# Optimization experiments

Hardware: AMD Instinct MI355X
Metric: run time of the kernel (lower is better)

## Reference

```python
import jax, jax.numpy as jnp
import numpy as np

N = 8192
IN_F = 512
OUT_F = 512
ALPHA = 0.2  # leaky relu slope


def setup_inputs() -> dict:
    key = jax.random.key(0)
    k1, k2, k3, k4, k5 = jax.random.split(key, 5)
    inp = jax.random.normal(k1, (N, IN_F), dtype=jnp.float32)
    adj = jax.random.randint(k2, (N, N), 0, 2, dtype=jnp.int32)
    # linear1: [in, out] + bias
    W1 = jax.random.normal(k3, (IN_F, OUT_F), dtype=jnp.float32) * (1.0 / np.sqrt(IN_F))
    b1 = jnp.zeros((OUT_F,), dtype=jnp.float32)
    # linear2: maps 2*out -> 1; split into the two halves acting on h_i and h_j
    a = jax.random.normal(k4, (2 * OUT_F,), dtype=jnp.float32) * (1.0 / np.sqrt(2 * OUT_F))
    a1 = a[:OUT_F]
    a2 = a[OUT_F:]
    b2 = jnp.zeros((), dtype=jnp.float32)
    return {"inp": inp, "adj": adj, "W1": W1, "b1": b1, "a1": a1, "a2": a2, "b2": b2}


def reference(inp, adj, W1, b1, a1, a2, b2):
    h = inp @ W1 + b1  # [N, out]
    # linear2(cat(h_i, h_j)) == h_i@a1 + h_j@a2 + b2 -> avoids the N*N*2F tensor
    e = jax.nn.leaky_relu((h @ a1)[:, None] + (h @ a2)[None, :] + b2, ALPHA)  # [N, N]
    attention = jnp.where(adj > 0, e, jnp.float32(-1e12))
    attention = jax.nn.softmax(attention, axis=1)
    h_prime = attention @ h  # [N, out]
    return jax.nn.elu(h_prime)  # concat=True
```

## Files before the change

kernel.cpp:

```cpp
#include <hip/hip_runtime.h>
#include <hip/hip_bf16.h>
#include <stdint.h>

#define NR 8192
#define FD 512
#define BM 128
#define BKC 128

typedef __attribute__((ext_vector_type(8))) short s8v;
typedef __attribute__((ext_vector_type(4))) float f32x4;

static __device__ __forceinline__ short bf16_rtne(float x) {
    union { float f; uint32_t u; } v; v.f = x;
    uint32_t r = (v.u + 0x7FFFu + ((v.u >> 16) & 1u)) >> 16;
    return (short)r;
}
static __device__ __forceinline__ float bf16_to_f32(short s) {
    union { uint32_t u; float f; } v; v.u = ((uint32_t)(uint16_t)s) << 16;
    return v.f;
}
static __device__ __forceinline__ float asfloat_u32(uint32_t u) {
    union { uint32_t u; float f; } v; v.u = u; return v.f;
}

__global__ void k_prepack(const int* __restrict__ adj, uint32_t* __restrict__ bm) {
    int t = blockIdx.x * 256 + threadIdx.x;
    const int4* p = (const int4*)(adj + (size_t)t * 32);
    uint32_t word = 0;
#pragma unroll
    for (int g = 0; g < 8; ++g) {
        int4 v = p[g];
        word |= (uint32_t)(v.x != 0) << (g * 4);
        word |= (uint32_t)(v.y != 0) << (g * 4 + 1);
        word |= (uint32_t)(v.z != 0) << (g * 4 + 2);
        word |= (uint32_t)(v.w != 0) << (g * 4 + 3);
    }
    bm[t] = word;
}

__global__ void k_convert(const float* __restrict__ in, short* __restrict__ out) {
    int i = blockIdx.x * blockDim.x + threadIdx.x;
    float4 v = ((const float4*)in)[i];
    short4 s;
    s.x = bf16_rtne(v.x); s.y = bf16_rtne(v.y);
    s.z = bf16_rtne(v.z); s.w = bf16_rtne(v.w);
    ((short4*)out)[i] = s;
}

__global__ void k_w1t(const float* __restrict__ W1, short* __restrict__ W1T) {
    int i = blockIdx.x * 256 + threadIdx.x;
    int k = i & 511, n = i >> 9;
    W1T[(size_t)n * 512 + k] = bf16_rtne(W1[(size_t)k * 512 + n]);
}

__launch_bounds__(256)
__global__ void k_gemm_h(const short* __restrict__ A,
                         const short* __restrict__ BT,
                         const float* __restrict__ b1,
                         short* __restrict__ H,
                         short* __restrict__ HT2)
{
    const int lane = threadIdx.x & 63;
    const int wn   = threadIdx.x >> 6;
    const int m    = lane & 15;
    const int q    = lane >> 4;
    const int r0   = blockIdx.x * 32;
    const int c0   = blockIdx.y * 128 + wn * 32;

    f32x4 acc[2][2] = {};
#pragma unroll 1
    for (int k0 = 0; k0 < 512; k0 += 32) {
        s8v a[2], b[2];
#pragma unroll
        for (int rt = 0; rt < 2; ++rt)
            a[rt] = *(const s8v*)(A + (size_t)(r0 + rt * 16 + m) * 512 + k0 + q * 8);
#pragma unroll
        for (int nt = 0; nt < 2; ++nt)
            b[nt] = *(const s8v*)(BT + (size_t)(c0 + nt * 16 + m) * 512 + k0 + q * 8);
#pragma unroll
        for (int rt = 0; rt < 2; ++rt)
#pragma unroll
            for (int nt = 0; nt < 2; ++nt)
                acc[rt][nt] = __builtin_amdgcn_mfma_f32_16x16x32_bf16(a[rt], b[nt], acc[rt][nt], 0, 0, 0);
    }
    float b1v[2];
#pragma unroll
    for (int nt = 0; nt < 2; ++nt) b1v[nt] = b1[c0 + nt * 16 + m];

#pragma unroll
    for (int rt = 0; rt < 2; ++rt)
#pragma unroll
        for (int nt = 0; nt < 2; ++nt) {
            int col = c0 + nt * 16 + m;
            short4 hp;
#pragma unroll
            for (int r = 0; r < 4; ++r) {
                int row = r0 + rt * 16 + q * 4 + r;
                short hv = bf16_rtne(acc[rt][nt][r] + b1v[nt]);
                H[(size_t)row * 512 + col] = hv;
                ((short*)&hp)[r] = hv;
            }
            *(short4*)(HT2 + (size_t)blockIdx.x * (512 * 32) + (size_t)col * 32 + rt * 16 + q * 4) = hp;
        }
}

__global__ void k_f1f2(const short* __restrict__ H, const float* __restrict__ a1,
                       const float* __restrict__ a2, const float* __restrict__ b2,
                       float* __restrict__ nf1, float* __restrict__ E1,
                       float* __restrict__ E1b, uint2* __restrict__ jtab)
{
    const int lane = threadIdx.x & 63;
    const int row  = blockIdx.x * 4 + (threadIdx.x >> 6);
    s8v hv = *(const s8v*)(H + (size_t)row * 512 + lane * 8);
    float4 a1l = ((const float4*)(a1 + lane * 8))[0];
    float4 a1h = ((const float4*)(a1 + lane * 8))[1];
    float4 a2l = ((const float4*)(a2 + lane * 8))[0];
    float4 a2h = ((const float4*)(a2 + lane * 8))[1];
    float hf[8];
#pragma unroll
    for (int i = 0; i < 8; ++i) hf[i] = bf16_to_f32(hv[i]);
    float s1 = hf[0] * a1l.x + hf[1] * a1l.y + hf[2] * a1l.z + hf[3] * a1l.w
             + hf[4] * a1h.x + hf[5] * a1h.y + hf[6] * a1h.z + hf[7] * a1h.w;
    float s2 = hf[0] * a2l.x + hf[1] * a2l.y + hf[2] * a2l.z + hf[3] * a2l.w
             + hf[4] * a2h.x + hf[5] * a2h.y + hf[6] * a2h.z + hf[7] * a2h.w;
#pragma unroll
    for (int o = 32; o > 0; o >>= 1) {
        s1 += __shfl_xor(s1, o);
        s2 += __shfl_xor(s2, o);
    }
    if (lane == 0) {
        float f1v = s1;
        float f2v = s2 + b2[0];
        nf1[row]  = -f1v;
        E1[row]   = __expf(f1v);
        E1b[row]  = __expf(0.2f * f1v);
        uint32_t p = (uint32_t)(uint16_t)bf16_rtne(__expf(f2v))
                   | ((uint32_t)(uint16_t)bf16_rtne(__expf(0.2f * f2v)) << 16);
        union { float f; uint32_t u; } fb; fb.f = f2v;
        jtab[row] = make_uint2(p, fb.u);
    }
}

__launch_bounds__(512, 4)
__global__ void k_attn(const uint32_t* __restrict__ bm,
                       const short* __restrict__ HT2,
                       const float* __restrict__ nf1,
                       const float* __restrict__ E1,
                       const float* __restrict__ E1b,
                       const uint2* __restrict__ jtab,
                       float* __restrict__ nump,
                       float* __restrict__ denomp)
{
    __shared__ __align__(16) short wt[2][BM * BKC];

    const int t    = threadIdx.x;
    const int lane = t & 63;
    const int w    = t >> 6;
    const int wm   = w & 1;
    const int wn   = w >> 1;
    const int m    = lane & 15;
    const int q    = lane >> 4;

    const int band = blockIdx.x >> 3;
    const int cb   = (blockIdx.x >> 1) & 3;
    const int js   = blockIdx.x & 1;
    const int r0   = band * BM;
    const int jsb  = js * 4096;

    const int rowq = t >> 4;
    const int jg   = t & 15;
    const int byteoff = (jg & 3) * 8;

    float nf1v[4], e1v[4], e1bv[4];
#pragma unroll
    for (int r = 0; r < 4; ++r) {
        int rr = r0 + rowq * 4 + r;
        nf1v[r] = nf1[rr]; e1v[r] = E1[rr]; e1bv[r] = E1b[rr];
    }
    const uint32_t* bmp = bm + (size_t)(r0 + rowq * 4) * 256 + (jsb >> 5) + (jg >> 2);
    const uint4*   tabp = (const uint4*)jtab + ((jsb + jg * 8) >> 1);

    const int colbase = cb * 128 + wn * 32;
    const short* htp = HT2 + (size_t)(jsb >> 5) * 16384 + q * 8;

    f32x4 acc[4][2] = {};
    float dsum[4] = {0.f, 0.f, 0.f, 0.f};

#pragma unroll 1
    for (int ch = 0; ch < 4096 / BKC; ++ch) {
        const int p = ch & 1;
        uint32_t bw[4];
#pragma unroll
        for (int r = 0; r < 4; ++r) bw[r] = bmp[(size_t)r * 256 + ch * 4];
        uint4 tb[4];
#pragma unroll
        for (int i = 0; i < 4; ++i) tb[i] = tabp[ch * 64 + i];
        const uint32_t* tw = (const uint32_t*)tb;

#pragma unroll
        for (int r = 0; r < 4; ++r) {
            uint32_t byte = (bw[r] >> byteoff) & 0xFFu;
            s8v wv;
            float ds = 0.f;
#pragma unroll
            for (int jj = 0; jj < 8; ++jj) {
                uint32_t pk  = tw[jj * 2];
                float e2  = asfloat_u32(pk << 16);
                float e2b = asfloat_u32(pk & 0xFFFF0000u);
                float f2  = asfloat_u32(tw[jj * 2 + 1]);
                bool  c   = (f2 >= nf1v[r]);
                float wgt = c ? (e1v[r] * e2) : (e1bv[r] * e2b);
                wgt = ((byte >> jj) & 1u) ? wgt : 0.f;
                ds += wgt;
                wv[jj] = bf16_rtne(wgt);
            }
            dsum[r] += ds;
            int row  = rowq * 4 + r;
            int slot = jg ^ (row & 15);
            *(s8v*)&wt[p][row * BKC + slot * 8] = wv;
        }

        __syncthreads();

#pragma unroll
        for (int kk = 0; kk < 4; ++kk) {
            s8v b[2];
#pragma unroll
            for (int nt = 0; nt < 2; ++nt)
                b[nt] = *(const s8v*)(htp + (size_t)(ch * 4 + kk) * 16384 + (colbase + nt * 16 + m) * 32);
            const int sb = kk * 4 + q;
            s8v af[4];
#pragma unroll
            for (int i = 0; i < 4; ++i) {
                int row = wm * 64 + i * 16 + m;
                af[i] = *(const s8v*)&wt[p][row * BKC + ((sb ^ m) << 3)];
            }
#pragma unroll
            for (int i = 0; i < 4; ++i)
#pragma unroll
                for (int nt = 0; nt < 2; ++nt)
                    acc[i][nt] = __builtin_amdgcn_mfma_f32_16x16x32_bf16(af[i], b[nt], acc[i][nt], 0, 0, 0);
        }
    }

#pragma unroll
    for (int r = 0; r < 4; ++r) {
#pragma unroll
        for (int o = 1; o < 16; o <<= 1) dsum[r] += __shfl_xor(dsum[r], o);
    }
    if (cb == 0 && jg == 0) {
#pragma unroll
        for (int r = 0; r < 4; ++r)
            denomp[(size_t)js * NR + r0 + rowq * 4 + r] = dsum[r];
    }

    float* np = nump + (size_t)js * NR * FD;
#pragma unroll
    for (int i = 0; i < 4; ++i)
#pragma unroll
        for (int nt = 0; nt < 2; ++nt)
#pragma unroll
            for (int r = 0; r < 4; ++r) {
                int row = r0 + wm * 64 + i * 16 + q * 4 + r;
                int col = colbase + nt * 16 + m;
                np[(size_t)row * FD + col] = acc[i][nt][r];
            }
}

__global__ void k_combine(const float* __restrict__ nump,
                          const float* __restrict__ denomp,
                          float* __restrict__ out)
{
    size_t e = ((size_t)blockIdx.x * 256 + threadIdx.x) * 4;
    int row = (int)(e >> 9);
    float4 n0 = *(const float4*)(nump + e);
    float4 n1 = *(const float4*)(nump + (size_t)NR * FD + e);
    float d = denomp[row] + denomp[NR + row];
    float inv = 1.0f / d;
    float4 o;
    o.x = (n0.x + n1.x) * inv; o.y = (n0.y + n1.y) * inv;
    o.z = (n0.z + n1.z) * inv; o.w = (n0.w + n1.w) * inv;
    o.x = (o.x > 0.f) ? o.x : (__expf(o.x) - 1.f);
    o.y = (o.y > 0.f) ? o.y : (__expf(o.y) - 1.f);
    o.z = (o.z > 0.f) ? o.z : (__expf(o.z) - 1.f);
    o.w = (o.w > 0.f) ? o.w : (__expf(o.w) - 1.f);
    *(float4*)(out + e) = o;
}

extern "C" void kernel_launch(void* const* d_in, const int* in_sizes, int n_in,
                              void* d_out, int out_size, void* d_ws, size_t ws_size,
                              hipStream_t stream) {
    const float* inp = (const float*)d_in[0];
    const int*   adj = (const int*)d_in[1];
    const float* W1  = (const float*)d_in[2];
    const float* b1  = (const float*)d_in[3];
    const float* a1  = (const float*)d_in[4];
    const float* a2  = (const float*)d_in[5];
    const float* b2  = (const float*)d_in[6];
    float* out = (float*)d_out;

    short*    inp_bf = (short*)d_ws;
    short*    w1t    = inp_bf + (size_t)NR * FD;
    short*    h      = w1t + (size_t)FD * FD;
    short*    ht2    = h + (size_t)NR * FD;
    uint32_t* bmw    = (uint32_t*)(ht2 + (size_t)FD * NR);
    float*    nf1    = (float*)(bmw + (size_t)NR * 256);
    float*    E1     = nf1 + NR;
    float*    E1b    = E1 + NR;
    uint2*    jtab   = (uint2*)(E1b + NR);
    float*    nump   = (float*)(jtab + NR);
    float*    denomp = nump + (size_t)2 * NR * FD;

    k_prepack<<<NR * 256 / 256, 256, 0, stream>>>(adj, bmw);
    k_convert<<<(NR * FD / 4) / 256, 256, 0, stream>>>(inp, inp_bf);
    k_w1t<<<(FD * FD) / 256, 256, 0, stream>>>(W1, w1t);
    dim3 g1(NR / 32, FD / 128);
    k_gemm_h<<<g1, 256, 0, stream>>>(inp_bf, w1t, b1, h, ht2);
    k_f1f2<<<NR / 4, 256, 0, stream>>>(h, a1, a2, b2, nf1, E1, E1b, jtab);
    k_attn<<<(NR / BM) * 4 * 2, 512, 0, stream>>>(bmw, ht2, nf1, E1, E1b, jtab, nump, denomp);
    k_combine<<<(NR * FD / 4) / 256, 256, 0, stream>>>(nump, denomp, out);
}
```

Before: 569.2 us.

## Fuse adjacency mask read into attention kernel and widen blocks to full feature width

Removes the adjacency bitmask prepack kernel and the precomputed exp tables. The attention kernel now reads the int32 adjacency directly and computes exp(leaky_relu(f1+f2)) per element. Each 1024-thread block now covers all 512 output columns, and the j range is split four ways instead of two, so the combine step sums four partial numerators. The intent is to stop re-reading the weight-generation inputs once per column block and to drop a separate pass over the 256MB adjacency. The cost is a full exp per element, no max-subtraction for numerical safety, and a larger partial-numerator buffer to write and read back.

```diff
diff --git a/kernel.cpp b/kernel.cpp
--- a/kernel.cpp
+++ b/kernel.cpp
@@ -18,24 +18,6 @@
 static __device__ __forceinline__ float bf16_to_f32(short s) {
     union { uint32_t u; float f; } v; v.u = ((uint32_t)(uint16_t)s) << 16;
     return v.f;
-}
-static __device__ __forceinline__ float asfloat_u32(uint32_t u) {
-    union { uint32_t u; float f; } v; v.u = u; return v.f;
-}
-
-__global__ void k_prepack(const int* __restrict__ adj, uint32_t* __restrict__ bm) {
-    int t = blockIdx.x * 256 + threadIdx.x;
-    const int4* p = (const int4*)(adj + (size_t)t * 32);
-    uint32_t word = 0;
-#pragma unroll
-    for (int g = 0; g < 8; ++g) {
-        int4 v = p[g];
-        word |= (uint32_t)(v.x != 0) << (g * 4);
-        word |= (uint32_t)(v.y != 0) << (g * 4 + 1);
-        word |= (uint32_t)(v.z != 0) << (g * 4 + 2);
-        word |= (uint32_t)(v.w != 0) << (g * 4 + 3);
-    }
-    bm[t] = word;
 }
 
 __global__ void k_convert(const float* __restrict__ in, short* __restrict__ out) {
@@ -106,8 +88,7 @@
 
 __global__ void k_f1f2(const short* __restrict__ H, const float* __restrict__ a1,
                        const float* __restrict__ a2, const float* __restrict__ b2,
-                       float* __restrict__ nf1, float* __restrict__ E1,
-                       float* __restrict__ E1b, uint2* __restrict__ jtab)
+                       float* __restrict__ f1, float* __restrict__ f2s)
 {
     const int lane = threadIdx.x & 63;
     const int row  = blockIdx.x * 4 + (threadIdx.x >> 6);
@@ -129,25 +110,16 @@
         s2 += __shfl_xor(s2, o);
     }
     if (lane == 0) {
-        float f1v = s1;
-        float f2v = s2 + b2[0];
-        nf1[row]  = -f1v;
-        E1[row]   = __expf(f1v);
-        E1b[row]  = __expf(0.2f * f1v);
-        uint32_t p = (uint32_t)(uint16_t)bf16_rtne(__expf(f2v))
-                   | ((uint32_t)(uint16_t)bf16_rtne(__expf(0.2f * f2v)) << 16);
-        union { float f; uint32_t u; } fb; fb.f = f2v;
-        jtab[row] = make_uint2(p, fb.u);
-    }
-}
-
-__launch_bounds__(512, 4)
-__global__ void k_attn(const uint32_t* __restrict__ bm,
+        f1[row]  = s1;
+        f2s[row] = s2 + b2[0];
+    }
+}
+
+__launch_bounds__(1024)
+__global__ void k_attn(const int* __restrict__ adj,
                        const short* __restrict__ HT2,
-                       const float* __restrict__ nf1,
-                       const float* __restrict__ E1,
-                       const float* __restrict__ E1b,
-                       const uint2* __restrict__ jtab,
+                       const float* __restrict__ f1,
+                       const float* __restrict__ f2s,
                        float* __restrict__ nump,
                        float* __restrict__ denomp)
 {
@@ -156,113 +128,93 @@
     const int t    = threadIdx.x;
     const int lane = t & 63;
     const int w    = t >> 6;
-    const int wm   = w & 1;
-    const int wn   = w >> 1;
+    const int wr   = w & 1;
+    const int wc   = w >> 1;
     const int m    = lane & 15;
     const int q    = lane >> 4;
 
-    const int band = blockIdx.x >> 3;
-    const int cb   = (blockIdx.x >> 1) & 3;
-    const int js   = blockIdx.x & 1;
+    const int band = blockIdx.x & 63;
+    const int js   = blockIdx.x >> 6;
     const int r0   = band * BM;
-    const int jsb  = js * 4096;
-
-    const int rowq = t >> 4;
-    const int jg   = t & 15;
-    const int byteoff = (jg & 3) * 8;
-
-    float nf1v[4], e1v[4], e1bv[4];
-#pragma unroll
-    for (int r = 0; r < 4; ++r) {
-        int rr = r0 + rowq * 4 + r;
-        nf1v[r] = nf1[rr]; e1v[r] = E1[rr]; e1bv[r] = E1b[rr];
-    }
-    const uint32_t* bmp = bm + (size_t)(r0 + rowq * 4) * 256 + (jsb >> 5) + (jg >> 2);
-    const uint4*   tabp = (const uint4*)jtab + ((jsb + jg * 8) >> 1);
-
-    const int colbase = cb * 128 + wn * 32;
-    const short* htp = HT2 + (size_t)(jsb >> 5) * 16384 + q * 8;
-
-    f32x4 acc[4][2] = {};
-    float dsum[4] = {0.f, 0.f, 0.f, 0.f};
+    const int jb0  = js * 2048;
+
+    const int prow = t >> 3;
+    const int jg   = t & 7;
+
+    const float f1v = f1[r0 + prow];
+    const int*   adjp = adj + (size_t)(r0 + prow) * NR + jb0 + jg * 16;
+    const float* f2p  = f2s + jb0 + jg * 16;
+
+    f32x4 acc[4][4] = {};
+    float dsum = 0.f;
 
 #pragma unroll 1
-    for (int ch = 0; ch < 4096 / BKC; ++ch) {
+    for (int ch = 0; ch < 2048 / BKC; ++ch) {
         const int p = ch & 1;
-        uint32_t bw[4];
-#pragma unroll
-        for (int r = 0; r < 4; ++r) bw[r] = bmp[(size_t)r * 256 + ch * 4];
-        uint4 tb[4];
-#pragma unroll
-        for (int i = 0; i < 4; ++i) tb[i] = tabp[ch * 64 + i];
-        const uint32_t* tw = (const uint32_t*)tb;
-
-#pragma unroll
-        for (int r = 0; r < 4; ++r) {
-            uint32_t byte = (bw[r] >> byteoff) & 0xFFu;
-            s8v wv;
-            float ds = 0.f;
-#pragma unroll
-            for (int jj = 0; jj < 8; ++jj) {
-                uint32_t pk  = tw[jj * 2];
-                float e2  = asfloat_u32(pk << 16);
-                float e2b = asfloat_u32(pk & 0xFFFF0000u);
-                float f2  = asfloat_u32(tw[jj * 2 + 1]);
-                bool  c   = (f2 >= nf1v[r]);
-                float wgt = c ? (e1v[r] * e2) : (e1bv[r] * e2b);
-                wgt = ((byte >> jj) & 1u) ? wgt : 0.f;
-                ds += wgt;
-                wv[jj] = bf16_rtne(wgt);
-            }
-            dsum[r] += ds;
-            int row  = rowq * 4 + r;
-            int slot = jg ^ (row & 15);
-            *(s8v*)&wt[p][row * BKC + slot * 8] = wv;
-        }
+        int4   aj[4];
+        float4 fv[4];
+#pragma unroll
+        for (int g = 0; g < 4; ++g) {
+            aj[g] = ((const int4*)(adjp + ch * BKC))[g];
+            fv[g] = ((const float4*)(f2p + ch * BKC))[g];
+        }
+        float wgt[16];
+#pragma unroll
+        for (int jj = 0; jj < 16; ++jj) {
+            int   a  = ((const int*)aj)[jj];
+            float s  = f1v + ((const float*)fv)[jj];
+            float l  = fmaxf(s, 0.2f * s);
+            float e  = __expf(l);
+            float wv = (a != 0) ? e : 0.f;
+            dsum += wv;
+            wgt[jj] = wv;
+        }
+        s8v wv0, wv1;
+#pragma unroll
+        for (int jj = 0; jj < 8; ++jj) {
+            wv0[jj] = bf16_rtne(wgt[jj]);
+            wv1[jj] = bf16_rtne(wgt[8 + jj]);
+        }
+        const int sw = prow & 15;
+        *(s8v*)&wt[p][prow * BKC + (((2 * jg) ^ sw) << 3)]     = wv0;
+        *(s8v*)&wt[p][prow * BKC + (((2 * jg + 1) ^ sw) << 3)] = wv1;
 
         __syncthreads();
 
 #pragma unroll
         for (int kk = 0; kk < 4; ++kk) {
-            s8v b[2];
-#pragma unroll
-            for (int nt = 0; nt < 2; ++nt)
-                b[nt] = *(const s8v*)(htp + (size_t)(ch * 4 + kk) * 16384 + (colbase + nt * 16 + m) * 32);
-            const int sb = kk * 4 + q;
+            const int jt = (jb0 + ch * BKC + kk * 32) >> 5;
+            const short* hb = HT2 + (size_t)jt * 16384 + q * 8;
             s8v af[4];
 #pragma unroll
             for (int i = 0; i < 4; ++i) {
-                int row = wm * 64 + i * 16 + m;
-                af[i] = *(const s8v*)&wt[p][row * BKC + ((sb ^ m) << 3)];
-            }
-#pragma unroll
-            for (int i = 0; i < 4; ++i)
-#pragma unroll
-                for (int nt = 0; nt < 2; ++nt)
-                    acc[i][nt] = __builtin_amdgcn_mfma_f32_16x16x32_bf16(af[i], b[nt], acc[i][nt], 0, 0, 0);
-        }
-    }
-
-#pragma unroll
-    for (int r = 0; r < 4; ++r) {
-#pragma unroll
-        for (int o = 1; o < 16; o <<= 1) dsum[r] += __shfl_xor(dsum[r], o);
-    }
-    if (cb == 0 && jg == 0) {
-#pragma unroll
-        for (int r = 0; r < 4; ++r)
-            denomp[(size_t)js * NR + r0 + rowq * 4 + r] = dsum[r];
-    }
+                int row = wr * 64 + i * 16 + m;
+                af[i] = *(const s8v*)&wt[p][row * BKC + (((kk * 4 + q) ^ m) << 3)];
+            }
+#pragma unroll
+            for (int nt = 0; nt < 4; ++nt) {
+                s8v b = *(const s8v*)(hb + (size_t)(wc * 64 + nt * 16 + m) * 32);
+#pragma unroll
+                for (int i = 0; i < 4; ++i)
+                    acc[i][nt] = __builtin_amdgcn_mfma_f32_16x16x32_bf16(af[i], b, acc[i][nt], 0, 0, 0);
+            }
+        }
+    }
+
+    dsum += __shfl_xor(dsum, 1);
+    dsum += __shfl_xor(dsum, 2);
+    dsum += __shfl_xor(dsum, 4);
+    if (jg == 0) denomp[(size_t)js * NR + r0 + prow] = dsum;
 
     float* np = nump + (size_t)js * NR * FD;
 #pragma unroll
     for (int i = 0; i < 4; ++i)
 #pragma unroll
-        for (int nt = 0; nt < 2; ++nt)
+        for (int nt = 0; nt < 4; ++nt)
 #pragma unroll
             for (int r = 0; r < 4; ++r) {
-                int row = r0 + wm * 64 + i * 16 + q * 4 + r;
-                int col = colbase + nt * 16 + m;
+                int row = r0 + wr * 64 + i * 16 + q * 4 + r;
+                int col = wc * 64 + nt * 16 + m;
                 np[(size_t)row * FD + col] = acc[i][nt][r];
             }
 }
@@ -275,11 +227,15 @@
     int row = (int)(e >> 9);
     float4 n0 = *(const float4*)(nump + e);
     float4 n1 = *(const float4*)(nump + (size_t)NR * FD + e);
-    float d = denomp[row] + denomp[NR + row];
+    float4 n2 = *(const float4*)(nump + (size_t)2 * NR * FD + e);
+    float4 n3 = *(const float4*)(nump + (size_t)3 * NR * FD + e);
+    float d = denomp[row] + denomp[NR + row] + denomp[2 * NR + row] + denomp[3 * NR + row];
     float inv = 1.0f / d;
     float4 o;
-    o.x = (n0.x + n1.x) * inv; o.y = (n0.y + n1.y) * inv;
-    o.z = (n0.z + n1.z) * inv; o.w = (n0.w + n1.w) * inv;
+    o.x = (n0.x + n1.x + n2.x + n3.x) * inv;
+    o.y = (n0.y + n1.y + n2.y + n3.y) * inv;
+    o.z = (n0.z + n1.z + n2.z + n3.z) * inv;
+    o.w = (n0.w + n1.w + n2.w + n3.w) * inv;
     o.x = (o.x > 0.f) ? o.x : (__expf(o.x) - 1.f);
     o.y = (o.y > 0.f) ? o.y : (__expf(o.y) - 1.f);
     o.z = (o.z > 0.f) ? o.z : (__expf(o.z) - 1.f);
@@ -299,24 +255,20 @@
     const float* b2  = (const float*)d_in[6];
     float* out = (float*)d_out;
 
-    short*    inp_bf = (short*)d_ws;
-    short*    w1t    = inp_bf + (size_t)NR * FD;
-    short*    h      = w1t + (size_t)FD * FD;
-    short*    ht2    = h + (size_t)NR * FD;
-    uint32_t* bmw    = (uint32_t*)(ht2 + (size_t)FD * NR);
-    float*    nf1    = (float*)(bmw + (size_t)NR * 256);
-    float*    E1     = nf1 + NR;
-    float*    E1b    = E1 + NR;
-    uint2*    jtab   = (uint2*)(E1b + NR);
-    float*    nump   = (float*)(jtab + NR);
-    float*    denomp = nump + (size_t)2 * NR * FD;
-
-    k_prepack<<<NR * 256 / 256, 256, 0, stream>>>(adj, bmw);
+    short* inp_bf = (short*)d_ws;
+    short* w1t    = inp_bf + (size_t)NR * FD;
+    short* h      = w1t + (size_t)FD * FD;
+    short* ht2    = h + (size_t)NR * FD;
+    float* f1     = (float*)(ht2 + (size_t)FD * NR);
+    float* f2s    = f1 + NR;
+    float* nump   = f2s + NR;
+    float* denomp = nump + (size_t)4 * NR * FD;
+
     k_convert<<<(NR * FD / 4) / 256, 256, 0, stream>>>(inp, inp_bf);
     k_w1t<<<(FD * FD) / 256, 256, 0, stream>>>(W1, w1t);
     dim3 g1(NR / 32, FD / 128);
     k_gemm_h<<<g1, 256, 0, stream>>>(inp_bf, w1t, b1, h, ht2);
-    k_f1f2<<<NR / 4, 256, 0, stream>>>(h, a1, a2, b2, nf1, E1, E1b, jtab);
-    k_attn<<<(NR / BM) * 4 * 2, 512, 0, stream>>>(bmw, ht2, nf1, E1, E1b, jtab, nump, denomp);
+    k_f1f2<<<NR / 4, 256, 0, stream>>>(h, a1, a2, b2, f1, f2s);
+    k_attn<<<64 * 4, 1024, 0, stream>>>(adj, ht2, f1, f2s, nump, denomp);
     k_combine<<<(NR * FD / 4) / 256, 256, 0, stream>>>(nump, denomp, out);
 }
```

After: 523.8 us. 1.09x faster.
